# Kernel tuning notes

Hardware: AMD Instinct MI355X
Metric: run time of the kernel (lower is better)

## Reference

```python
import itertools
import jax, jax.numpy as jnp
import numpy as np

GRID_SIZE = (8, 8)
B, C, T, M = 16, 306, 4096, 270


def setup_inputs() -> dict:
    key = jax.random.key(0)
    kx, kp, kw = jax.random.split(key, 3)
    x = jax.random.normal(kx, (B, C, T), dtype=jnp.float32)
    # positions in [-1, 0.74] keeps ceil index < grid_size (the original torch
    # code goes out of bounds for positions at/near +1)
    positions = jax.random.uniform(kp, (B, C, 2), dtype=jnp.float32,
                                   minval=-1.0, maxval=0.74)
    grid_weights = jax.random.normal(kw, (M, int(np.prod(GRID_SIZE))), dtype=jnp.float32)
    return {"x": x, "positions": positions, "grid_weights": grid_weights}


def reference(x, positions, grid_weights):
    # x: [B, C, T], positions: [B, C, D], grid_weights: [M, G]
    gs = jnp.asarray(GRID_SIZE, dtype=x.dtype)
    D = len(GRID_SIZE)
    G = int(np.prod(GRID_SIZE))
    strides = [int(np.prod(GRID_SIZE[d + 1:])) for d in range(D)]

    grid_pos = (positions + 1.0) * gs / 2.0       # [B, C, D] in [0, grid_size)
    low = jnp.floor(grid_pos)
    idx_low = low.astype(jnp.int32)               # [B, C, D]
    idx_high = jnp.ceil(grid_pos).astype(jnp.int32)
    w_high = grid_pos - low                       # fractional part
    w_low = 1.0 - w_high

    b_idx = jnp.arange(x.shape[0])[:, None]       # [B, 1] batch index for scatter
    grid_values = jnp.zeros((x.shape[0], G, x.shape[2]), dtype=x.dtype)

    # 2^D = 4 corners: multilinear interpolation scatter-add into flat grid
    for combo in itertools.product((0, 1), repeat=D):
        idx = jnp.zeros(idx_low.shape[:-1], dtype=jnp.int32)
        w = jnp.ones(w_low.shape[:-1], dtype=x.dtype)
        for d, hi in enumerate(combo):
            idx = idx + (idx_high if hi else idx_low)[..., d] * strides[d]
            w = w * (w_high if hi else w_low)[..., d]
        grid_values = grid_values.at[b_idx, idx].add(x * w[..., None])

    # [M, G] x [B, G, T] -> [B, M, T]
    return jnp.einsum('mg,bgt->bmt', grid_weights, grid_values)
```

## Files before the change

### kernel.cpp

```cpp
#include <hip/hip_runtime.h>
#include <cstdint>

#define B_   16
#define C_   306
#define T_   4096
#define M_   270
#define G_   64
#define MT_  17
#define KB_  10
#define TT   64
#define BDIM 256
#define NW   4

typedef __attribute__((ext_vector_type(8))) short s8;
typedef __attribute__((ext_vector_type(4))) float f4;
typedef __attribute__((ext_vector_type(4))) int   i4;

__device__ __forceinline__ short f2bf(float f) {
    unsigned u = __builtin_bit_cast(unsigned, f);
    u += 0x7FFFu + ((u >> 16) & 1u);
    return (short)(u >> 16);
}
__device__ __forceinline__ float bf2f(short h) {
    return __builtin_bit_cast(float, ((unsigned)(unsigned short)h) << 16);
}

__global__ __launch_bounds__(BDIM) void a_build(const float* __restrict__ pos,
                                                const float* __restrict__ gw,
                                                i4* __restrict__ Ah,
                                                i4* __restrict__ Al) {
    __shared__ float At[16][321];
    const int mt  = blockIdx.x;
    const int b   = blockIdx.y;
    const int tid = threadIdx.x;
    const int mr  = tid & 15;
    const int cg  = tid >> 4;
    const int m   = mt * 16 + mr;

    for (int c = cg; c < KB_ * 32; c += 16) {
        float v = 0.0f;
        if (c < C_ && m < M_) {
            const float* pp = pos + ((size_t)b * C_ + c) * 2;
            float gp0 = (pp[0] + 1.0f) * 4.0f;
            float gp1 = (pp[1] + 1.0f) * 4.0f;
            float f0 = floorf(gp0), f1 = floorf(gp1);
            int l0 = (int)f0, l1 = (int)f1;
            int h0 = (int)ceilf(gp0), h1 = (int)ceilf(gp1);
            float wh0 = gp0 - f0, wh1 = gp1 - f1;
            float wl0 = 1.0f - wh0, wl1 = 1.0f - wh1;
            const float* wm = gw + (size_t)m * G_;
            v = wl0 * wl1 * wm[l0 * 8 + l1] + wl0 * wh1 * wm[l0 * 8 + h1]
              + wh0 * wl1 * wm[h0 * 8 + l1] + wh0 * wh1 * wm[h0 * 8 + h1];
        }
        At[mr][c] = v;
    }
    __syncthreads();

    const int lane = tid & 63;
    const int mr2  = lane & 15;
    const int j0   = (lane >> 4) * 8;
    for (int kb = tid >> 6; kb < KB_; kb += 4) {
        s8 hv, lv;
        #pragma unroll
        for (int j = 0; j < 8; ++j) {
            float v = At[mr2][kb * 32 + j0 + j];
            short h = f2bf(v);
            hv[j] = h;
            lv[j] = f2bf(v - bf2f(h));
        }
        const int idx = ((b * MT_ + mt) * KB_ + kb) * 64 + lane;
        Ah[idx] = __builtin_bit_cast(i4, hv);
        Al[idx] = __builtin_bit_cast(i4, lv);
    }
}

__global__ __launch_bounds__(BDIM, 2) void gemm_kernel(
    const float* __restrict__ x, const i4* __restrict__ Ahp,
    const i4* __restrict__ Alp, float* __restrict__ out) {
    __shared__ s8 BhT[2][320];
    __shared__ s8 BlT[2][320];

    const int orig = blockIdx.y * gridDim.x + blockIdx.x;
    const int xcd  = orig & 7;
    const int nbid = xcd * 128 + (orig >> 3);
    const int b    = nbid >> 6;
    const int t0   = (nbid & 63) * TT;

    const int tid  = threadIdx.x;
    const int lane = tid & 63;
    const int wave = __builtin_amdgcn_readfirstlane(tid >> 6);
    const int quad = lane >> 4;
    const int lcol = lane & 15;
    const int col  = tid & 63;

    const float* xrow = x + (size_t)b * C_ * T_ + t0 + col;
    const i4* Abase_h = Ahp + (size_t)(b * MT_ * KB_) * 64 + lane;
    const i4* Abase_l = Alp + (size_t)(b * MT_ * KB_) * 64 + lane;

    float rv[2][8];
    s8 ah[2][5], al[2][5];

    #pragma unroll
    for (int mi = 0; mi < 5; ++mi) {
        const int mt = wave + mi * NW;
        if (mt < MT_) {
            ah[0][mi] = __builtin_bit_cast(s8, Abase_h[(mt * KB_) * 64]);
            al[0][mi] = __builtin_bit_cast(s8, Abase_l[(mt * KB_) * 64]);
        }
    }
    #pragma unroll
    for (int j = 0; j < 8; ++j)
        rv[0][j] = xrow[(size_t)(8 * wave + j) * T_];
    #pragma unroll
    for (int j = 0; j < 8; ++j)
        rv[1][j] = xrow[(size_t)(32 + 8 * wave + j) * T_];

    {
        s8 hv, lv;
        #pragma unroll
        for (int j = 0; j < 8; ++j) {
            short h = f2bf(rv[0][j]);
            hv[j] = h;
            lv[j] = f2bf(rv[0][j] - bf2f(h));
        }
        BhT[0][col * 5 + wave] = hv;
        BlT[0][col * 5 + wave] = lv;
    }

    f4 acc[5][4];
    #pragma unroll
    for (int mi = 0; mi < 5; ++mi)
        #pragma unroll
        for (int nt = 0; nt < 4; ++nt)
            acc[mi][nt] = (f4){0.f, 0.f, 0.f, 0.f};

    asm volatile("s_waitcnt lgkmcnt(0)" ::: "memory");
    __builtin_amdgcn_sched_barrier(0);
    __builtin_amdgcn_s_barrier();
    __builtin_amdgcn_sched_barrier(0);

    #pragma unroll
    for (int kb = 0; kb < KB_; ++kb) {
        const int cur = kb & 1;
        const int nxt = cur ^ 1;

        if (kb + 1 < KB_) {
            #pragma unroll
            for (int mi = 0; mi < 5; ++mi) {
                const int mt = wave + mi * NW;
                if (mt < MT_) {
                    const int idx = (mt * KB_ + kb + 1) * 64;
                    ah[nxt][mi] = __builtin_bit_cast(s8, Abase_h[idx]);
                    al[nxt][mi] = __builtin_bit_cast(s8, Abase_l[idx]);
                }
            }
        }

        if (kb + 2 < KB_) {
            #pragma unroll
            for (int j = 0; j < 8; ++j) {
                const int c0 = (kb + 2) * 32 + 8 * wave + j;
                rv[cur][j] = (c0 < C_) ? xrow[(size_t)c0 * T_] : 0.0f;
            }
        }

        s8 bh[4], bl[4];
        #pragma unroll
        for (int nt = 0; nt < 4; ++nt) {
            bh[nt] = BhT[cur][(nt * 16 + lcol) * 5 + quad];
            bl[nt] = BlT[cur][(nt * 16 + lcol) * 5 + quad];
        }

        #pragma unroll
        for (int mi = 0; mi < 5; ++mi) {
            const int mt = wave + mi * NW;
            if (mt < MT_) {
                #pragma unroll
                for (int nt = 0; nt < 4; ++nt) {
                    f4 a = acc[mi][nt];
                    a = __builtin_amdgcn_mfma_f32_16x16x32_bf16(al[cur][mi], bh[nt], a, 0, 0, 0);
                    a = __builtin_amdgcn_mfma_f32_16x16x32_bf16(ah[cur][mi], bl[nt], a, 0, 0, 0);
                    a = __builtin_amdgcn_mfma_f32_16x16x32_bf16(ah[cur][mi], bh[nt], a, 0, 0, 0);
                    acc[mi][nt] = a;
                }
            }
        }

        if (kb + 1 < KB_) {
            s8 hv, lv;
            #pragma unroll
            for (int j = 0; j < 8; ++j) {
                short h = f2bf(rv[nxt][j]);
                hv[j] = h;
                lv[j] = f2bf(rv[nxt][j] - bf2f(h));
            }
            BhT[nxt][col * 5 + wave] = hv;
            BlT[nxt][col * 5 + wave] = lv;

            asm volatile("s_waitcnt lgkmcnt(0)" ::: "memory");
            __builtin_amdgcn_sched_barrier(0);
            __builtin_amdgcn_s_barrier();
            __builtin_amdgcn_sched_barrier(0);
        }
    }

    float* op = out + (size_t)b * M_ * T_ + t0;
    #pragma unroll
    for (int mi = 0; mi < 5; ++mi) {
        const int mt = wave + mi * NW;
        if (mt < MT_) {
            const int mrow = mt * 16 + quad * 4;
            #pragma unroll
            for (int nt = 0; nt < 4; ++nt) {
                #pragma unroll
                for (int r = 0; r < 4; ++r) {
                    const int m = mrow + r;
                    if (m < M_)
                        op[(size_t)m * T_ + nt * 16 + lcol] = acc[mi][nt][r];
                }
            }
        }
    }
}

extern "C" void kernel_launch(void* const* d_in, const int* in_sizes, int n_in,
                              void* d_out, int out_size, void* d_ws, size_t ws_size,
                              hipStream_t stream) {
    const float* x   = (const float*)d_in[0];
    const float* pos = (const float*)d_in[1];
    const float* gw  = (const float*)d_in[2];
    float* out = (float*)d_out;

    i4* Ah = (i4*)d_ws;
    i4* Al = (i4*)((char*)d_ws + 2785280);

    a_build<<<dim3(MT_, B_), BDIM, 0, stream>>>(pos, gw, Ah, Al);

    dim3 grid(T_ / TT, B_);
    gemm_kernel<<<grid, BDIM, 0, stream>>>(x, Ah, Al, out);
}
```

Before: 180.8 us.

## Stage K dimension in two halves of five blocks with fewer barriers

Replaces the per-32-channel double-buffered loop, which had one barrier per K block, with two phases of five K blocks each. The first half of x is loaded, converted and staged in shared memory up front. The second half is prefetched into registers while the first half computes, then staged after one barrier. A fragments are now loaded inline instead of being prefetched one step ahead. This cuts the barrier count from nine to about three, at the cost of more registers (40 extra floats held for x), a larger shared buffer and less overlap of A loads, which may hurt occupancy under launch_bounds(256,2).

```diff
diff --git a/kernel.cpp b/kernel.cpp
--- a/kernel.cpp
+++ b/kernel.cpp
@@ -77,8 +77,8 @@
 __global__ __launch_bounds__(BDIM, 2) void gemm_kernel(
     const float* __restrict__ x, const i4* __restrict__ Ahp,
     const i4* __restrict__ Alp, float* __restrict__ out) {
-    __shared__ s8 BhT[2][320];
-    __shared__ s8 BlT[2][320];
+    __shared__ s8 BhT[5][320];
+    __shared__ s8 BlT[5][320];
 
     const int orig = blockIdx.y * gridDim.x + blockIdx.x;
     const int xcd  = orig & 7;
@@ -97,35 +97,34 @@
     const i4* Abase_h = Ahp + (size_t)(b * MT_ * KB_) * 64 + lane;
     const i4* Abase_l = Alp + (size_t)(b * MT_ * KB_) * 64 + lane;
 
-    float rv[2][8];
-    s8 ah[2][5], al[2][5];
-
-    #pragma unroll
-    for (int mi = 0; mi < 5; ++mi) {
-        const int mt = wave + mi * NW;
-        if (mt < MT_) {
-            ah[0][mi] = __builtin_bit_cast(s8, Abase_h[(mt * KB_) * 64]);
-            al[0][mi] = __builtin_bit_cast(s8, Abase_l[(mt * KB_) * 64]);
-        }
-    }
-    #pragma unroll
-    for (int j = 0; j < 8; ++j)
-        rv[0][j] = xrow[(size_t)(8 * wave + j) * T_];
-    #pragma unroll
-    for (int j = 0; j < 8; ++j)
-        rv[1][j] = xrow[(size_t)(32 + 8 * wave + j) * T_];
-
-    {
+    float rv[5][8];
+    #pragma unroll
+    for (int k5 = 0; k5 < 5; ++k5)
+        #pragma unroll
+        for (int j = 0; j < 8; ++j)
+            rv[k5][j] = xrow[(size_t)(k5 * 32 + 8 * wave + j) * T_];
+
+    #pragma unroll
+    for (int k5 = 0; k5 < 5; ++k5) {
         s8 hv, lv;
         #pragma unroll
         for (int j = 0; j < 8; ++j) {
-            short h = f2bf(rv[0][j]);
+            short h = f2bf(rv[k5][j]);
             hv[j] = h;
-            lv[j] = f2bf(rv[0][j] - bf2f(h));
-        }
-        BhT[0][col * 5 + wave] = hv;
-        BlT[0][col * 5 + wave] = lv;
-    }
+            lv[j] = f2bf(rv[k5][j] - bf2f(h));
+        }
+        BhT[k5][col * 5 + wave] = hv;
+        BlT[k5][col * 5 + wave] = lv;
+    }
+
+    float rw[5][8];
+    #pragma unroll
+    for (int k5 = 0; k5 < 5; ++k5)
+        #pragma unroll
+        for (int j = 0; j < 8; ++j) {
+            const int c0 = 160 + k5 * 32 + 8 * wave + j;
+            rw[k5][j] = (c0 < C_) ? xrow[(size_t)c0 * T_] : 0.0f;
+        }
 
     f4 acc[5][4];
     #pragma unroll
@@ -140,67 +139,79 @@
     __builtin_amdgcn_sched_barrier(0);
 
     #pragma unroll
-    for (int kb = 0; kb < KB_; ++kb) {
-        const int cur = kb & 1;
-        const int nxt = cur ^ 1;
-
-        if (kb + 1 < KB_) {
-            #pragma unroll
-            for (int mi = 0; mi < 5; ++mi) {
-                const int mt = wave + mi * NW;
-                if (mt < MT_) {
-                    const int idx = (mt * KB_ + kb + 1) * 64;
-                    ah[nxt][mi] = __builtin_bit_cast(s8, Abase_h[idx]);
-                    al[nxt][mi] = __builtin_bit_cast(s8, Abase_l[idx]);
-                }
-            }
-        }
-
-        if (kb + 2 < KB_) {
-            #pragma unroll
-            for (int j = 0; j < 8; ++j) {
-                const int c0 = (kb + 2) * 32 + 8 * wave + j;
-                rv[cur][j] = (c0 < C_) ? xrow[(size_t)c0 * T_] : 0.0f;
-            }
-        }
-
+    for (int k5 = 0; k5 < 5; ++k5) {
         s8 bh[4], bl[4];
         #pragma unroll
         for (int nt = 0; nt < 4; ++nt) {
-            bh[nt] = BhT[cur][(nt * 16 + lcol) * 5 + quad];
-            bl[nt] = BlT[cur][(nt * 16 + lcol) * 5 + quad];
-        }
-
+            bh[nt] = BhT[k5][(nt * 16 + lcol) * 5 + quad];
+            bl[nt] = BlT[k5][(nt * 16 + lcol) * 5 + quad];
+        }
         #pragma unroll
         for (int mi = 0; mi < 5; ++mi) {
             const int mt = wave + mi * NW;
             if (mt < MT_) {
+                const int idx = (mt * KB_ + k5) * 64;
+                const s8 ah = __builtin_bit_cast(s8, Abase_h[idx]);
+                const s8 al = __builtin_bit_cast(s8, Abase_l[idx]);
                 #pragma unroll
                 for (int nt = 0; nt < 4; ++nt) {
                     f4 a = acc[mi][nt];
-                    a = __builtin_amdgcn_mfma_f32_16x16x32_bf16(al[cur][mi], bh[nt], a, 0, 0, 0);
-                    a = __builtin_amdgcn_mfma_f32_16x16x32_bf16(ah[cur][mi], bl[nt], a, 0, 0, 0);
-                    a = __builtin_amdgcn_mfma_f32_16x16x32_bf16(ah[cur][mi], bh[nt], a, 0, 0, 0);
+                    a = __builtin_amdgcn_mfma_f32_16x16x32_bf16(al, bh[nt], a, 0, 0, 0);
+                    a = __builtin_amdgcn_mfma_f32_16x16x32_bf16(ah, bl[nt], a, 0, 0, 0);
+                    a = __builtin_amdgcn_mfma_f32_16x16x32_bf16(ah, bh[nt], a, 0, 0, 0);
                     acc[mi][nt] = a;
                 }
             }
         }
-
-        if (kb + 1 < KB_) {
-            s8 hv, lv;
-            #pragma unroll
-            for (int j = 0; j < 8; ++j) {
-                short h = f2bf(rv[nxt][j]);
-                hv[j] = h;
-                lv[j] = f2bf(rv[nxt][j] - bf2f(h));
+    }
+
+    asm volatile("s_waitcnt lgkmcnt(0)" ::: "memory");
+    __builtin_amdgcn_sched_barrier(0);
+    __builtin_amdgcn_s_barrier();
+    __builtin_amdgcn_sched_barrier(0);
+
+    #pragma unroll
+    for (int k5 = 0; k5 < 5; ++k5) {
+        s8 hv, lv;
+        #pragma unroll
+        for (int j = 0; j < 8; ++j) {
+            short h = f2bf(rw[k5][j]);
+            hv[j] = h;
+            lv[j] = f2bf(rw[k5][j] - bf2f(h));
+        }
+        BhT[k5][col * 5 + wave] = hv;
+        BlT[k5][col * 5 + wave] = lv;
+    }
+
+    asm volatile("s_waitcnt lgkmcnt(0)" ::: "memory");
+    __builtin_amdgcn_sched_barrier(0);
+    __builtin_amdgcn_s_barrier();
+    __builtin_amdgcn_sched_barrier(0);
+
+    #pragma unroll
+    for (int k5 = 0; k5 < 5; ++k5) {
+        s8 bh[4], bl[4];
+        #pragma unroll
+        for (int nt = 0; nt < 4; ++nt) {
+            bh[nt] = BhT[k5][(nt * 16 + lcol) * 5 + quad];
+            bl[nt] = BlT[k5][(nt * 16 + lcol) * 5 + quad];
+        }
+        #pragma unroll
+        for (int mi = 0; mi < 5; ++mi) {
+            const int mt = wave + mi * NW;
+            if (mt < MT_) {
+                const int idx = (mt * KB_ + 5 + k5) * 64;
+                const s8 ah = __builtin_bit_cast(s8, Abase_h[idx]);
+                const s8 al = __builtin_bit_cast(s8, Abase_l[idx]);
+                #pragma unroll
+                for (int nt = 0; nt < 4; ++nt) {
+                    f4 a = acc[mi][nt];
+                    a = __builtin_amdgcn_mfma_f32_16x16x32_bf16(al, bh[nt], a, 0, 0, 0);
+                    a = __builtin_amdgcn_mfma_f32_16x16x32_bf16(ah, bl[nt], a, 0, 0, 0);
+                    a = __builtin_amdgcn_mfma_f32_16x16x32_bf16(ah, bh[nt], a, 0, 0, 0);
+                    acc[mi][nt] = a;
+                }
             }
-            BhT[nxt][col * 5 + wave] = hv;
-            BlT[nxt][col * 5 + wave] = lv;
-
-            asm volatile("s_waitcnt lgkmcnt(0)" ::: "memory");
-            __builtin_amdgcn_sched_barrier(0);
-            __builtin_amdgcn_s_barrier();
-            __builtin_amdgcn_sched_barrier(0);
         }
     }
 
```

Result: slower. 212.8 us (+17.7%).

## Split GEMM M dimension across two blocks per time tile to raise occupancy

Applied to the files above, without the earlier changes.

Each time tile is now handled by two blocks, each owning about half of the 17 M-tiles (9 and 8). Per-thread accumulators and A fragments shrink from 5 to 3 M-tiles, and launch bounds rise to 3 blocks per CU, which should cut register pressure and double the grid to improve latency hiding. The cost is that each block reloads and reconverts its x tile into bf16 hi/lo, so x global reads and conversion work double, and some waves are idle in the last M slot.

```diff
diff --git a/kernel.cpp b/kernel.cpp
--- a/kernel.cpp
+++ b/kernel.cpp
@@ -11,6 +11,7 @@
 #define TT   64
 #define BDIM 256
 #define NW   4
+#define MIH  3
 
 typedef __attribute__((ext_vector_type(8))) short s8;
 typedef __attribute__((ext_vector_type(4))) float f4;
@@ -74,7 +75,7 @@
     }
 }
 
-__global__ __launch_bounds__(BDIM, 2) void gemm_kernel(
+__global__ __launch_bounds__(BDIM, 3) void gemm_kernel(
     const float* __restrict__ x, const i4* __restrict__ Ahp,
     const i4* __restrict__ Alp, float* __restrict__ out) {
     __shared__ s8 BhT[2][320];
@@ -82,9 +83,13 @@
 
     const int orig = blockIdx.y * gridDim.x + blockIdx.x;
     const int xcd  = orig & 7;
-    const int nbid = xcd * 128 + (orig >> 3);
-    const int b    = nbid >> 6;
-    const int t0   = (nbid & 63) * TT;
+    const int nbid = xcd * 256 + (orig >> 3);
+    const int b    = nbid >> 7;
+    const int r    = nbid & 127;
+    const int t0   = (r >> 1) * TT;
+    const int half = r & 1;
+    const int mbase = half * 9;
+    const int NMT   = half ? 8 : 9;
 
     const int tid  = threadIdx.x;
     const int lane = tid & 63;
@@ -98,12 +103,13 @@
     const i4* Abase_l = Alp + (size_t)(b * MT_ * KB_) * 64 + lane;
 
     float rv[2][8];
-    s8 ah[2][5], al[2][5];
-
-    #pragma unroll
-    for (int mi = 0; mi < 5; ++mi) {
-        const int mt = wave + mi * NW;
-        if (mt < MT_) {
+    s8 ah[2][MIH], al[2][MIH];
+
+    #pragma unroll
+    for (int mi = 0; mi < MIH; ++mi) {
+        const int ml = wave + mi * NW;
+        if (ml < NMT) {
+            const int mt = mbase + ml;
             ah[0][mi] = __builtin_bit_cast(s8, Abase_h[(mt * KB_) * 64]);
             al[0][mi] = __builtin_bit_cast(s8, Abase_l[(mt * KB_) * 64]);
         }
@@ -127,9 +133,9 @@
         BlT[0][col * 5 + wave] = lv;
     }
 
-    f4 acc[5][4];
-    #pragma unroll
-    for (int mi = 0; mi < 5; ++mi)
+    f4 acc[MIH][4];
+    #pragma unroll
+    for (int mi = 0; mi < MIH; ++mi)
         #pragma unroll
         for (int nt = 0; nt < 4; ++nt)
             acc[mi][nt] = (f4){0.f, 0.f, 0.f, 0.f};
@@ -146,10 +152,10 @@
 
         if (kb + 1 < KB_) {
             #pragma unroll
-            for (int mi = 0; mi < 5; ++mi) {
-                const int mt = wave + mi * NW;
-                if (mt < MT_) {
-                    const int idx = (mt * KB_ + kb + 1) * 64;
+            for (int mi = 0; mi < MIH; ++mi) {
+                const int ml = wave + mi * NW;
+                if (ml < NMT) {
+                    const int idx = ((mbase + ml) * KB_ + kb + 1) * 64;
                     ah[nxt][mi] = __builtin_bit_cast(s8, Abase_h[idx]);
                     al[nxt][mi] = __builtin_bit_cast(s8, Abase_l[idx]);
                 }
@@ -172,9 +178,9 @@
         }
 
         #pragma unroll
-        for (int mi = 0; mi < 5; ++mi) {
-            const int mt = wave + mi * NW;
-            if (mt < MT_) {
+        for (int mi = 0; mi < MIH; ++mi) {
+            const int ml = wave + mi * NW;
+            if (ml < NMT) {
                 #pragma unroll
                 for (int nt = 0; nt < 4; ++nt) {
                     f4 a = acc[mi][nt];
@@ -206,17 +212,17 @@
 
     float* op = out + (size_t)b * M_ * T_ + t0;
     #pragma unroll
-    for (int mi = 0; mi < 5; ++mi) {
-        const int mt = wave + mi * NW;
-        if (mt < MT_) {
-            const int mrow = mt * 16 + quad * 4;
+    for (int mi = 0; mi < MIH; ++mi) {
+        const int ml = wave + mi * NW;
+        if (ml < NMT) {
+            const int mrow = (mbase + ml) * 16 + quad * 4;
             #pragma unroll
             for (int nt = 0; nt < 4; ++nt) {
                 #pragma unroll
-                for (int r = 0; r < 4; ++r) {
-                    const int m = mrow + r;
+                for (int rr = 0; rr < 4; ++rr) {
+                    const int m = mrow + rr;
                     if (m < M_)
-                        op[(size_t)m * T_ + nt * 16 + lcol] = acc[mi][nt][r];
+                        op[(size_t)m * T_ + nt * 16 + lcol] = acc[mi][nt][rr];
                 }
             }
         }
@@ -236,6 +242,6 @@
 
     a_build<<<dim3(MT_, B_), BDIM, 0, stream>>>(pos, gw, Ah, Al);
 
-    dim3 grid(T_ / TT, B_);
+    dim3 grid(128, 16);
     gemm_kernel<<<grid, BDIM, 0, stream>>>(x, Ah, Al, out);
 }
```

New measurement: 190.1 us. 1.05x slower.
